# Optimization experiments

Measured on AMD Instinct MI355X. Metric: run time of the kernel, lower is better.

## Reference

```python
import jax, jax.numpy as jnp
import numpy as np

N = 50000      # nodes
E = 800000     # edges
F_IN = 128     # input node features
HID = 96       # hidden_channels (heads=1 -> in_dim=HID)
L = 4          # num_layers
OUT = 1
EPS_SM = 1e-16 # PyG softmax eps


def layer_norm(x, g, b):
    mu = jnp.mean(x, axis=-1, keepdims=True)
    var = jnp.var(x, axis=-1, keepdims=True)
    return (x - mu) * jax.lax.rsqrt(var + 1e-5) * g + b


def gatv2_layer(h, src, dst, ea, Wl, bl, Wr, br, We, att, bias):
    # GATv2Conv, heads=1, concat=True, add_self_loops=False, edge_dim=1
    xl = h @ Wl + bl                      # [N, C] source transform (x_j)
    xr = h @ Wr + br                      # [N, C] target transform (x_i)
    e = xl[src] + xr[dst] + ea @ We       # [E, C]
    e = jax.nn.leaky_relu(e, 0.2)
    alpha = e @ att                       # [E]
    # softmax over incoming edges of each destination node
    m = jax.ops.segment_max(alpha, dst, num_segments=N)
    a = jnp.exp(alpha - m[dst])
    s = jax.ops.segment_sum(a, dst, num_segments=N)
    a = a / (s[dst] + EPS_SM)
    out = jax.ops.segment_sum(xl[src] * a[:, None], dst, num_segments=N)
    return out + bias


def setup_inputs() -> dict:
    key = jax.random.key(0)
    ks = jax.random.split(key, 24)
    sc_in = 1.0 / np.sqrt(F_IN)
    sc_h = 1.0 / np.sqrt(HID)
    inp = {
        "x": jax.random.normal(ks[0], (N, F_IN), jnp.float32),
        "edge_index": jax.random.randint(ks[1], (2, E), 0, N, jnp.int64),
        "edge_weight": jax.random.uniform(ks[2], (E,), jnp.float32),
        "enc_W": jax.random.normal(ks[3], (F_IN, HID), jnp.float32) * sc_in,
        "enc_b": jnp.zeros((HID,), jnp.float32),
        "Wl": jax.random.normal(ks[4], (L, HID, HID), jnp.float32) * sc_h,
        "bl": jnp.zeros((L, HID), jnp.float32),
        "Wr": jax.random.normal(ks[5], (L, HID, HID), jnp.float32) * sc_h,
        "br": jnp.zeros((L, HID), jnp.float32),
        "We": jax.random.normal(ks[6], (L, 1, HID), jnp.float32),
        "att": jax.random.normal(ks[7], (L, HID), jnp.float32) * sc_h,
        "bias": jnp.zeros((L, HID), jnp.float32),
        "ln_g": jnp.ones((L, HID), jnp.float32),
        "ln_b": jnp.zeros((L, HID), jnp.float32),
        "lnf_g": jnp.ones((HID,), jnp.float32),
        "lnf_b": jnp.zeros((HID,), jnp.float32),
        "fc_W": jax.random.normal(ks[8], (HID, OUT), jnp.float32) * sc_h,
        "fc_b": jnp.zeros((OUT,), jnp.float32),
    }
    return inp


def reference(x, edge_index, edge_weight, enc_W, enc_b, Wl, bl, Wr, br, We, att,
              bias, ln_g, ln_b, lnf_g, lnf_b, fc_W, fc_b):
    src, dst = edge_index[0], edge_index[1]
    ea = edge_weight[:, None]             # [E, 1] edge_attr
    h = x @ enc_W + enc_b                 # node encoder
    for i in range(L):                    # DeepGCNLayer block='res+'
        hn = jax.nn.relu(layer_norm(h, ln_g[i], ln_b[i]))
        h = h + gatv2_layer(hn, src, dst, ea, Wl[i], bl[i], Wr[i], br[i],
                            We[i], att[i], bias[i])
    h = jax.nn.relu(layer_norm(h, lnf_g, lnf_b))
    return h @ fc_W + fc_b
```

## Files before the change

kernel.cpp:

```cpp
#include <hip/hip_runtime.h>
#include <math.h>

#define NN 50000
#define EE 800000
#define FIN 128
#define HID 96
#define NL 4
#define CHUNK 1024

typedef __attribute__((ext_vector_type(8))) short short8;
typedef __attribute__((ext_vector_type(4))) float floatx4;
typedef __attribute__((ext_vector_type(2))) _Float16 half2v;

__device__ __forceinline__ float wave_sum(float v) {
    #pragma unroll
    for (int off = 32; off > 0; off >>= 1) v += __shfl_xor(v, off);
    return v;
}

__device__ __forceinline__ unsigned short f32_to_bf16_rne(float x) {
    unsigned u = __float_as_uint(x);
    unsigned r = (u + 0x7FFFu + ((u >> 16) & 1u)) >> 16;
    return (unsigned short)r;
}
__device__ __forceinline__ float bf16_to_f32(unsigned short h) {
    return __uint_as_float(((unsigned)h) << 16);
}
__device__ __forceinline__ void split2(float a, float b, unsigned& hi, unsigned& lo) {
    unsigned short ha = f32_to_bf16_rne(a), hb = f32_to_bf16_rne(b);
    unsigned short la = f32_to_bf16_rne(a - bf16_to_f32(ha));
    unsigned short lb = f32_to_bf16_rne(b - bf16_to_f32(hb));
    hi = (unsigned)ha | ((unsigned)hb << 16);
    lo = (unsigned)la | ((unsigned)lb << 16);
}

__global__ void k_hist(const int* __restrict__ dst, int* __restrict__ deg, int E) {
    int e = blockIdx.x * blockDim.x + threadIdx.x;
    if (e < E) atomicAdd(&deg[dst[e]], 1);
}

__global__ void k_scan1(const int* __restrict__ deg, int* __restrict__ partials, int n) {
    __shared__ int lds[256];
    int t = threadIdx.x;
    int base = blockIdx.x * CHUNK + t * 4;
    int s = 0;
    #pragma unroll
    for (int q = 0; q < 4; q++) { int idx = base + q; if (idx < n) s += deg[idx]; }
    lds[t] = s; __syncthreads();
    for (int o = 128; o > 0; o >>= 1) { if (t < o) lds[t] += lds[t + o]; __syncthreads(); }
    if (t == 0) partials[blockIdx.x] = lds[0];
}

__global__ void k_scan_mid(int* partials, int nb, int* rowptr, int n) {
    int lane = threadIdx.x;
    int orig = (lane < nb) ? partials[lane] : 0;
    int v = orig;
    #pragma unroll
    for (int off = 1; off < 64; off <<= 1) {
        int u = __shfl_up(v, off);
        if (lane >= off) v += u;
    }
    if (lane < nb) partials[lane] = v - orig;
    if (lane == 63) rowptr[n] = v;
}

__global__ void k_scan3(const int* __restrict__ deg, const int* __restrict__ partials,
                        int* __restrict__ rowptr, int* __restrict__ cursor, int n) {
    __shared__ int lds[256];
    int t = threadIdx.x;
    int base = blockIdx.x * CHUNK + t * 4;
    int v[4];
    #pragma unroll
    for (int q = 0; q < 4; q++) { int idx = base + q; v[q] = (idx < n) ? deg[idx] : 0; }
    int tsum = v[0] + v[1] + v[2] + v[3];
    lds[t] = tsum; __syncthreads();
    for (int o = 1; o < 256; o <<= 1) {
        int add = (t >= o) ? lds[t - o] : 0;
        __syncthreads();
        lds[t] += add;
        __syncthreads();
    }
    int excl = lds[t] - tsum;
    int run = partials[blockIdx.x] + excl;
    #pragma unroll
    for (int q = 0; q < 4; q++) {
        int idx = base + q;
        if (idx < n) { rowptr[idx] = run; cursor[idx] = run; run += v[q]; }
    }
}

__global__ void k_scatter(const int* __restrict__ src, const int* __restrict__ dst,
                          const float* __restrict__ ew, int* __restrict__ cursor,
                          uint2* __restrict__ epack, int E) {
    int e = blockIdx.x * blockDim.x + threadIdx.x;
    if (e < E) {
        int p = atomicAdd(&cursor[dst[e]], 1);
        epack[p] = make_uint2((unsigned)src[e], __float_as_uint(ew[e]));
    }
}

__global__ void k_wprep(const float* __restrict__ Wl, const float* __restrict__ Wr,
                        unsigned short* __restrict__ wf_hi, unsigned short* __restrict__ wf_lo) {
    int t = blockIdx.x * blockDim.x + threadIdx.x;
    if (t >= NL * 2 * 9216) return;
    int within = t % 9216, pair = t / 9216;
    int lr = pair & 1, layer = pair >> 1;
    int j = within & 7;
    int lane = (within >> 3) & 63;
    int cs = within >> 9;
    int s = cs % 3, ct = cs / 3;
    int col = ct * 16 + (lane & 15);
    int k = s * 32 + (lane >> 4) * 8 + j;
    const float* W = (lr ? Wr : Wl) + (size_t)layer * HID * HID;
    float v = W[k * HID + col];
    unsigned short hi = f32_to_bf16_rne(v);
    wf_hi[t] = hi;
    wf_lo[t] = f32_to_bf16_rne(v - bf16_to_f32(hi));
}

__global__ void k_wprep_enc(const float* __restrict__ W,
                            unsigned short* __restrict__ we_hi, unsigned short* __restrict__ we_lo) {
    int t = blockIdx.x * blockDim.x + threadIdx.x;
    if (t >= 12288) return;
    int j = t & 7;
    int lane = (t >> 3) & 63;
    int cs = t >> 9;
    int s = cs & 3, ct = cs >> 2;
    int col = ct * 16 + (lane & 15);
    int k = s * 32 + (lane >> 4) * 8 + j;
    float v = W[k * HID + col];
    unsigned short hi = f32_to_bf16_rne(v);
    we_hi[t] = hi;
    we_lo[t] = f32_to_bf16_rne(v - bf16_to_f32(hi));
}

__global__ __launch_bounds__(256) void k_enc_mfma(const float* __restrict__ x,
        const unsigned short* __restrict__ we_hi, const unsigned short* __restrict__ we_lo,
        const float* __restrict__ b, float* __restrict__ h, int n) {
    int t = threadIdx.x;
    int wave = t >> 6, lane = t & 63;
    int quad = lane >> 4, lid = lane & 15;
    int r0 = blockIdx.x * 64 + wave * 16;
    int arow = r0 + lid; if (arow >= n) arow = n - 1;
    short8 aH[4], aL[4];
    #pragma unroll
    for (int s = 0; s < 4; s++) {
        float4 p0 = *(const float4*)(x + (size_t)arow * FIN + s * 32 + quad * 8);
        float4 p1 = *(const float4*)(x + (size_t)arow * FIN + s * 32 + quad * 8 + 4);
        float f[8] = {p0.x, p0.y, p0.z, p0.w, p1.x, p1.y, p1.z, p1.w};
        #pragma unroll
        for (int j = 0; j < 8; j++) {
            unsigned short hi = f32_to_bf16_rne(f[j]);
            aH[s][j] = (short)hi;
            aL[s][j] = (short)f32_to_bf16_rne(f[j] - bf16_to_f32(hi));
        }
    }
    #pragma unroll
    for (int ct = 0; ct < 6; ct++) {
        floatx4 acc = {0.f, 0.f, 0.f, 0.f};
        #pragma unroll
        for (int s = 0; s < 4; s++) {
            short8 bH = *(const short8*)(we_hi + ((ct * 4 + s) * 64 + lane) * 8);
            short8 bL = *(const short8*)(we_lo + ((ct * 4 + s) * 64 + lane) * 8);
            acc = __builtin_amdgcn_mfma_f32_16x16x32_bf16(aH[s], bH, acc, 0, 0, 0);
            acc = __builtin_amdgcn_mfma_f32_16x16x32_bf16(aH[s], bL, acc, 0, 0, 0);
            acc = __builtin_amdgcn_mfma_f32_16x16x32_bf16(aL[s], bH, acc, 0, 0, 0);
        }
        int col = ct * 16 + lid;
        float bv = b[col];
        #pragma unroll
        for (int rg = 0; rg < 4; rg++) {
            int orow = r0 + quad * 4 + rg;
            if (orow < n) h[(size_t)orow * HID + col] = acc[rg] + bv;
        }
    }
}

__global__ __launch_bounds__(256) void k_gemm2_mfma(
        const unsigned short* __restrict__ hn_hi, const unsigned short* __restrict__ hn_lo,
        const unsigned short* __restrict__ wf_hi, const unsigned short* __restrict__ wf_lo,
        const float* __restrict__ bl, const float* __restrict__ br,
        unsigned short* __restrict__ xl_h, float* __restrict__ xr, int n) {
    __shared__ unsigned short lh[9216];
    __shared__ unsigned short ll[9216];
    int t = threadIdx.x;
    int wave = t >> 6, lane = t & 63;
    int quad = lane >> 4, lid = lane & 15;
    int r0 = blockIdx.x * 64 + wave * 16;
    int arow = r0 + lid; if (arow >= n) arow = n - 1;
    short8 aH[3], aL[3];
    #pragma unroll
    for (int s = 0; s < 3; s++) {
        aH[s] = *(const short8*)(hn_hi + (size_t)arow * HID + s * 32 + quad * 8);
        aL[s] = *(const short8*)(hn_lo + (size_t)arow * HID + s * 32 + quad * 8);
    }
    for (int lr = 0; lr < 2; lr++) {
        const unsigned short* sh = wf_hi + lr * 9216;
        const unsigned short* sl = wf_lo + lr * 9216;
        __syncthreads();
        for (int u = t; u < 1152; u += 256) {
            *(short8*)(lh + u * 8) = *(const short8*)(sh + u * 8);
            *(short8*)(ll + u * 8) = *(const short8*)(sl + u * 8);
        }
        __syncthreads();
        const float* bias = lr ? br : bl;
        #pragma unroll
        for (int ct = 0; ct < 6; ct++) {
            floatx4 acc = {0.f, 0.f, 0.f, 0.f};
            #pragma unroll
            for (int s = 0; s < 3; s++) {
                short8 bH = *(const short8*)(lh + ((ct * 3 + s) * 64 + lane) * 8);
                short8 bL = *(const short8*)(ll + ((ct * 3 + s) * 64 + lane) * 8);
                acc = __builtin_amdgcn_mfma_f32_16x16x32_bf16(aH[s], bH, acc, 0, 0, 0);
                acc = __builtin_amdgcn_mfma_f32_16x16x32_bf16(aH[s], bL, acc, 0, 0, 0);
                acc = __builtin_amdgcn_mfma_f32_16x16x32_bf16(aL[s], bH, acc, 0, 0, 0);
            }
            int col = ct * 16 + lid;
            float bv = bias[col];
            #pragma unroll
            for (int rg = 0; rg < 4; rg++) {
                int orow = r0 + quad * 4 + rg;
                if (orow < n) {
                    float o = acc[rg] + bv;
                    if (lr == 0) {
                        _Float16 hv = (_Float16)o;
                        xl_h[(size_t)orow * HID + col] = *(unsigned short*)&hv;
                    } else {
                        xr[(size_t)orow * HID + col] = o;
                    }
                }
            }
        }
    }
}

__global__ __launch_bounds__(256) void k_ln_relu(const float* __restrict__ h, const float* __restrict__ g,
                                                 const float* __restrict__ bt,
                                                 unsigned short* __restrict__ hn_hi,
                                                 unsigned short* __restrict__ hn_lo, int n) {
    int lane = threadIdx.x & 63;
    int node = blockIdx.x * 4 + (threadIdx.x >> 6);
    if (node >= n) return;
    bool act = lane < 48;
    int d = lane * 2;
    float2 x2 = make_float2(0.f, 0.f);
    if (act) x2 = *(const float2*)(h + (size_t)node * HID + d);
    float s  = wave_sum(x2.x + x2.y);
    float sq = wave_sum(x2.x * x2.x + x2.y * x2.y);
    float mu = s * (1.f / 96.f);
    float var = sq * (1.f / 96.f) - mu * mu;
    float rs = rsqrtf(var + 1e-5f);
    if (act) {
        float2 g2 = *(const float2*)(g + d);
        float2 b2 = *(const float2*)(bt + d);
        float ox = fmaxf((x2.x - mu) * rs * g2.x + b2.x, 0.f);
        float oy = fmaxf((x2.y - mu) * rs * g2.y + b2.y, 0.f);
        unsigned hi, lo;
        split2(ox, oy, hi, lo);
        *(unsigned*)(hn_hi + (size_t)node * HID + d) = hi;
        *(unsigned*)(hn_lo + (size_t)node * HID + d) = lo;
    }
}

__global__ __launch_bounds__(256) void k_gat_fused(
        const unsigned short* __restrict__ xl_h, const float* __restrict__ xr,
        const uint2* __restrict__ ep, const int* __restrict__ rowptr,
        const float* __restrict__ We, const float* __restrict__ att, const float* __restrict__ bias,
        float* __restrict__ h,
        unsigned short* __restrict__ hn_hi, unsigned short* __restrict__ hn_lo,
        float* __restrict__ out_final,
        const float* __restrict__ g, const float* __restrict__ bt,
        const float* __restrict__ fcW, const float* __restrict__ fcb,
        int mode, int n) {
    int lane = threadIdx.x & 63;
    int node = blockIdx.x * 4 + (threadIdx.x >> 6);
    if (node >= n) return;
    int grp = lane >> 4, sub = lane & 15;
    bool act = sub < 12;
    int d0 = sub * 8;
    unsigned gOffB = (unsigned)((act ? sub : 11) * 16);

    half2v we_h[4], at_h[4], xr_h[4];
    if (act) {
        float4 a0 = *(const float4*)(We + d0),  a1 = *(const float4*)(We + d0 + 4);
        float4 c0 = *(const float4*)(att + d0), c1 = *(const float4*)(att + d0 + 4);
        float4 r0 = *(const float4*)(xr + (size_t)node * HID + d0);
        float4 r1 = *(const float4*)(xr + (size_t)node * HID + d0 + 4);
        we_h[0] = half2v{(_Float16)a0.x, (_Float16)a0.y}; we_h[1] = half2v{(_Float16)a0.z, (_Float16)a0.w};
        we_h[2] = half2v{(_Float16)a1.x, (_Float16)a1.y}; we_h[3] = half2v{(_Float16)a1.z, (_Float16)a1.w};
        at_h[0] = half2v{(_Float16)c0.x, (_Float16)c0.y}; at_h[1] = half2v{(_Float16)c0.z, (_Float16)c0.w};
        at_h[2] = half2v{(_Float16)c1.x, (_Float16)c1.y}; at_h[3] = half2v{(_Float16)c1.z, (_Float16)c1.w};
        xr_h[0] = half2v{(_Float16)r0.x, (_Float16)r0.y}; xr_h[1] = half2v{(_Float16)r0.z, (_Float16)r0.w};
        xr_h[2] = half2v{(_Float16)r1.x, (_Float16)r1.y}; xr_h[3] = half2v{(_Float16)r1.z, (_Float16)r1.w};
    } else {
        #pragma unroll
        for (int j = 0; j < 4; j++) {
            we_h[j] = half2v{(_Float16)0.f, (_Float16)0.f};
            at_h[j] = we_h[j]; xr_h[j] = we_h[j];
        }
    }
    const half2v c02 = half2v{(_Float16)0.2f, (_Float16)0.2f};

    int beg = rowptr[node], end = rowptr[node + 1];
    float ssum = 0.f;
    float acc[8];
    #pragma unroll
    for (int j = 0; j < 8; j++) acc[j] = 0.f;

    union U8 { uint4 u; half2v h2[4]; _Float16 hf[8]; };

    auto lq = [&](int p, uint4& vraw, float& w, bool& val) {
        int pe = p + grp;
        val = pe < end;
        int pc = val ? pe : end - 1;
        uint2 e = ep[pc];
        w = __uint_as_float(e.y);
        vraw = *(const uint4*)((const char*)xl_h + (e.x * 192u + gOffB));
    };
    auto proc = [&](const uint4& vraw, float w, bool val) {
        U8 cv; cv.u = vraw;
        _Float16 wh = (_Float16)w;
        half2v w2 = half2v{wh, wh};
        float q = 0.f;
        #pragma unroll
        for (int j = 0; j < 4; j++) {
            half2v t = cv.h2[j] + xr_h[j];
            t = w2 * we_h[j] + t;
            half2v t2 = t * c02;
            t = __builtin_elementwise_max(t, t2);
#if __has_builtin(__builtin_amdgcn_fdot2)
            q = __builtin_amdgcn_fdot2(t, at_h[j], q, false);
#else
            q = fmaf((float)t[0], (float)at_h[j][0], q);
            q = fmaf((float)t[1], (float)at_h[j][1], q);
#endif
        }
        q += __shfl_xor(q, 1); q += __shfl_xor(q, 2);
        q += __shfl_xor(q, 4); q += __shfl_xor(q, 8);
        float e = val ? __expf(q) : 0.f;
        ssum += e;
        #pragma unroll
        for (int j = 0; j < 8; j++) acc[j] = fmaf((float)cv.hf[j], e, acc[j]);
    };

    if (beg < end) {
        uint4 vA, vB; float wA, wB; bool okA, okB;
        lq(beg,     vA, wA, okA);
        lq(beg + 4, vB, wB, okB);
        for (int p = beg; p < end; p += 8) {
            proc(vA, wA, okA);
            lq(p + 8, vA, wA, okA);
            proc(vB, wB, okB);
            lq(p + 12, vB, wB, okB);
        }
    }

    ssum += __shfl_xor(ssum, 16); ssum += __shfl_xor(ssum, 32);
    #pragma unroll
    for (int j = 0; j < 8; j++) {
        acc[j] += __shfl_xor(acc[j], 16);
        acc[j] += __shfl_xor(acc[j], 32);
    }
    float inv = 1.f / (ssum + 1e-16f);

    float nh[8];
    float s1 = 0.f, s2 = 0.f;
    if (act) {
        float4 h0 = *(const float4*)(h + (size_t)node * HID + d0);
        float4 h1 = *(const float4*)(h + (size_t)node * HID + d0 + 4);
        float4 b0 = *(const float4*)(bias + d0);
        float4 b1 = *(const float4*)(bias + d0 + 4);
        float hv[8] = {h0.x,h0.y,h0.z,h0.w,h1.x,h1.y,h1.z,h1.w};
        float bv[8] = {b0.x,b0.y,b0.z,b0.w,b1.x,b1.y,b1.z,b1.w};
        #pragma unroll
        for (int j = 0; j < 8; j++) {
            nh[j] = hv[j] + acc[j] * inv + bv[j];
            s1 += nh[j];
            s2 += nh[j] * nh[j];
        }
    } else {
        #pragma unroll
        for (int j = 0; j < 8; j++) nh[j] = 0.f;
    }
    #pragma unroll
    for (int off = 1; off < 16; off <<= 1) {
        s1 += __shfl_xor(s1, off);
        s2 += __shfl_xor(s2, off);
    }
    float mu = s1 * (1.f / 96.f);
    float var = s2 * (1.f / 96.f) - mu * mu;
    float rs = rsqrtf(var + 1e-5f);

    if (mode == 0) {
        if (grp == 0 && act) {
            float4 g0 = *(const float4*)(g + d0),  g1 = *(const float4*)(g + d0 + 4);
            float4 t0 = *(const float4*)(bt + d0), t1 = *(const float4*)(bt + d0 + 4);
            float gv[8] = {g0.x,g0.y,g0.z,g0.w,g1.x,g1.y,g1.z,g1.w};
            float tv[8] = {t0.x,t0.y,t0.z,t0.w,t1.x,t1.y,t1.z,t1.w};
            *(float4*)(h + (size_t)node * HID + d0)     = make_float4(nh[0], nh[1], nh[2], nh[3]);
            *(float4*)(h + (size_t)node * HID + d0 + 4) = make_float4(nh[4], nh[5], nh[6], nh[7]);
            unsigned hi[4], lo[4];
            #pragma unroll
            for (int j = 0; j < 4; j++) {
                float ox = fmaxf((nh[2*j]   - mu) * rs * gv[2*j]   + tv[2*j],   0.f);
                float oy = fmaxf((nh[2*j+1] - mu) * rs * gv[2*j+1] + tv[2*j+1], 0.f);
                split2(ox, oy, hi[j], lo[j]);
            }
            *(uint4*)(hn_hi + (size_t)node * HID + d0) = make_uint4(hi[0], hi[1], hi[2], hi[3]);
            *(uint4*)(hn_lo + (size_t)node * HID + d0) = make_uint4(lo[0], lo[1], lo[2], lo[3]);
        }
    } else {
        float pacc = 0.f;
        if (act) {
            float4 g0 = *(const float4*)(g + d0),  g1 = *(const float4*)(g + d0 + 4);
            float4 t0 = *(const float4*)(bt + d0), t1 = *(const float4*)(bt + d0 + 4);
            float4 w0 = *(const float4*)(fcW + d0), w1 = *(const float4*)(fcW + d0 + 4);
            float gv[8] = {g0.x,g0.y,g0.z,g0.w,g1.x,g1.y,g1.z,g1.w};
            float tv[8] = {t0.x,t0.y,t0.z,t0.w,t1.x,t1.y,t1.z,t1.w};
            float wv[8] = {w0.x,w0.y,w0.z,w0.w,w1.x,w1.y,w1.z,w1.w};
            #pragma unroll
            for (int j = 0; j < 8; j++) {
                float y = fmaxf((nh[j] - mu) * rs * gv[j] + tv[j], 0.f);
                pacc = fmaf(y, wv[j], pacc);
            }
        }
        #pragma unroll
        for (int off = 1; off < 16; off <<= 1) pacc += __shfl_xor(pacc, off);
        if (lane == 0) out_final[node] = pacc + fcb[0];
    }
}

extern "C" void kernel_launch(void* const* d_in, const int* in_sizes, int n_in,
                              void* d_out, int out_size, void* d_ws, size_t ws_size,
                              hipStream_t stream) {
    const float* x    = (const float*)d_in[0];
    const int*   ei   = (const int*)  d_in[1];
    const float* ew   = (const float*)d_in[2];
    const float* encW = (const float*)d_in[3];
    const float* encB = (const float*)d_in[4];
    const float* Wl   = (const float*)d_in[5];
    const float* bl   = (const float*)d_in[6];
    const float* Wr   = (const float*)d_in[7];
    const float* br   = (const float*)d_in[8];
    const float* We   = (const float*)d_in[9];
    const float* att  = (const float*)d_in[10];
    const float* bias = (const float*)d_in[11];
    const float* lng  = (const float*)d_in[12];
    const float* lnb  = (const float*)d_in[13];
    const float* lnfg = (const float*)d_in[14];
    const float* lnfb = (const float*)d_in[15];
    const float* fcW  = (const float*)d_in[16];
    const float* fcb  = (const float*)d_in[17];
    float* out = (float*)d_out;

    const int* src = ei;
    const int* dst = ei + EE;

    char* ws = (char*)d_ws;
    size_t off = 0;
    auto alloc = [&](size_t bytes) -> void* {
        void* p = ws + off;
        off += (bytes + 255) & ~(size_t)255;
        return p;
    };
    float* h      = (float*)alloc((size_t)NN * HID * 4);
    float* xr     = (float*)alloc((size_t)NN * HID * 4);
    unsigned short* xl_h  = (unsigned short*)alloc((size_t)NN * HID * 2 + 256);
    unsigned short* hn_hi = (unsigned short*)alloc((size_t)NN * HID * 2);
    unsigned short* hn_lo = (unsigned short*)alloc((size_t)NN * HID * 2);
    unsigned short* wf_hi = (unsigned short*)alloc((size_t)NL * 2 * 9216 * 2);
    unsigned short* wf_lo = (unsigned short*)alloc((size_t)NL * 2 * 9216 * 2);
    unsigned short* we_hi = (unsigned short*)alloc(12288 * 2);
    unsigned short* we_lo = (unsigned short*)alloc(12288 * 2);
    int*   deg    = (int*)  alloc((size_t)NN * 4);
    int*   rowptr = (int*)  alloc((size_t)(NN + 1) * 4);
    int*   cursor = (int*)  alloc((size_t)NN * 4);
    uint2* epack  = (uint2*)alloc((size_t)EE * 8);
    int*   parts  = (int*)  alloc(256 * 4);

    const int NB = (NN + CHUNK - 1) / CHUNK;
    const int EB = (EE + 255) / 256;
    const int MB = (NN + 63) / 64;
    const int WB = (NN + 3) / 4;

    hipMemsetAsync(deg, 0, (size_t)NN * 4, stream);
    k_hist<<<EB, 256, 0, stream>>>(dst, deg, EE);
    k_scan1<<<NB, 256, 0, stream>>>(deg, parts, NN);
    k_scan_mid<<<1, 64, 0, stream>>>(parts, NB, rowptr, NN);
    k_scan3<<<NB, 256, 0, stream>>>(deg, parts, rowptr, cursor, NN);
    k_scatter<<<EB, 256, 0, stream>>>(src, dst, ew, cursor, epack, EE);

    k_wprep<<<(NL * 2 * 9216 + 255) / 256, 256, 0, stream>>>(Wl, Wr, wf_hi, wf_lo);
    k_wprep_enc<<<(12288 + 255) / 256, 256, 0, stream>>>(encW, we_hi, we_lo);

    k_enc_mfma<<<MB, 256, 0, stream>>>(x, we_hi, we_lo, encB, h, NN);
    k_ln_relu<<<WB, 256, 0, stream>>>(h, lng, lnb, hn_hi, hn_lo, NN);

    for (int l = 0; l < NL; l++) {
        k_gemm2_mfma<<<MB, 256, 0, stream>>>(hn_hi, hn_lo,
            wf_hi + (size_t)l * 2 * 9216, wf_lo + (size_t)l * 2 * 9216,
            bl + l * HID, br + l * HID, xl_h, xr, NN);
        if (l < NL - 1) {
            k_gat_fused<<<WB, 256, 0, stream>>>(xl_h, xr, epack, rowptr,
                We + l * HID, att + l * HID, bias + l * HID,
                h, hn_hi, hn_lo, (float*)nullptr,
                lng + (l + 1) * HID, lnb + (l + 1) * HID,
                (const float*)nullptr, (const float*)nullptr, 0, NN);
        } else {
            k_gat_fused<<<WB, 256, 0, stream>>>(xl_h, xr, epack, rowptr,
                We + l * HID, att + l * HID, bias + l * HID,
                h, (unsigned short*)nullptr, (unsigned short*)nullptr, out,
                lnfg, lnfb, fcW, fcb, 1, NN);
        }
    }
}
```

Before: 503.7 us.

## Fuse first LayerNorm into encoder GEMM, store xr in fp16, use exp2

Folds the first LayerNorm+ReLU and bf16 hi/lo split into the encoder MFMA epilogue, computing row stats with 16-lane shuffles and dropping the separate k_ln_relu launch and its re-read of h. The gemm now writes the target transform xr as fp16 rather than fp32, halving that buffer's write and read traffic, and the GAT kernel loads it with one 16-byte load. The attention vector is pre-scaled by log2(e) so the softmax can use exp2f. Risks are extra fp16 rounding on xr and scattered 2-byte stores in the fused encoder epilogue.

```diff
diff --git a/kernel.cpp b/kernel.cpp
--- a/kernel.cpp
+++ b/kernel.cpp
@@ -25,13 +25,6 @@
 }
 __device__ __forceinline__ float bf16_to_f32(unsigned short h) {
     return __uint_as_float(((unsigned)h) << 16);
-}
-__device__ __forceinline__ void split2(float a, float b, unsigned& hi, unsigned& lo) {
-    unsigned short ha = f32_to_bf16_rne(a), hb = f32_to_bf16_rne(b);
-    unsigned short la = f32_to_bf16_rne(a - bf16_to_f32(ha));
-    unsigned short lb = f32_to_bf16_rne(b - bf16_to_f32(hb));
-    hi = (unsigned)ha | ((unsigned)hb << 16);
-    lo = (unsigned)la | ((unsigned)lb << 16);
 }
 
 __global__ void k_hist(const int* __restrict__ dst, int* __restrict__ deg, int E) {
@@ -136,7 +129,10 @@
 
 __global__ __launch_bounds__(256) void k_enc_mfma(const float* __restrict__ x,
         const unsigned short* __restrict__ we_hi, const unsigned short* __restrict__ we_lo,
-        const float* __restrict__ b, float* __restrict__ h, int n) {
+        const float* __restrict__ b,
+        const float* __restrict__ lng, const float* __restrict__ lnb,
+        float* __restrict__ h,
+        unsigned short* __restrict__ hn_hi, unsigned short* __restrict__ hn_lo, int n) {
     int t = threadIdx.x;
     int wave = t >> 6, lane = t & 63;
     int quad = lane >> 4, lid = lane & 15;
@@ -155,6 +151,7 @@
             aL[s][j] = (short)f32_to_bf16_rne(f[j] - bf16_to_f32(hi));
         }
     }
+    floatx4 o[6];
     #pragma unroll
     for (int ct = 0; ct < 6; ct++) {
         floatx4 acc = {0.f, 0.f, 0.f, 0.f};
@@ -166,12 +163,35 @@
             acc = __builtin_amdgcn_mfma_f32_16x16x32_bf16(aH[s], bL, acc, 0, 0, 0);
             acc = __builtin_amdgcn_mfma_f32_16x16x32_bf16(aL[s], bH, acc, 0, 0, 0);
         }
-        int col = ct * 16 + lid;
-        float bv = b[col];
-        #pragma unroll
-        for (int rg = 0; rg < 4; rg++) {
-            int orow = r0 + quad * 4 + rg;
-            if (orow < n) h[(size_t)orow * HID + col] = acc[rg] + bv;
+        float bv = b[ct * 16 + lid];
+        #pragma unroll
+        for (int rg = 0; rg < 4; rg++) o[ct][rg] = acc[rg] + bv;
+    }
+    #pragma unroll
+    for (int rg = 0; rg < 4; rg++) {
+        float s1 = 0.f, s2 = 0.f;
+        #pragma unroll
+        for (int ct = 0; ct < 6; ct++) { s1 += o[ct][rg]; s2 += o[ct][rg] * o[ct][rg]; }
+        #pragma unroll
+        for (int off = 1; off < 16; off <<= 1) {
+            s1 += __shfl_xor(s1, off);
+            s2 += __shfl_xor(s2, off);
+        }
+        float mu = s1 * (1.f / 96.f);
+        float var = s2 * (1.f / 96.f) - mu * mu;
+        float rs = rsqrtf(var + 1e-5f);
+        int orow = r0 + quad * 4 + rg;
+        if (orow < n) {
+            #pragma unroll
+            for (int ct = 0; ct < 6; ct++) {
+                int col = ct * 16 + lid;
+                float v = o[ct][rg];
+                h[(size_t)orow * HID + col] = v;
+                float y = fmaxf((v - mu) * rs * lng[col] + lnb[col], 0.f);
+                unsigned short hi = f32_to_bf16_rne(y);
+                hn_hi[(size_t)orow * HID + col] = hi;
+                hn_lo[(size_t)orow * HID + col] = f32_to_bf16_rne(y - bf16_to_f32(hi));
+            }
         }
     }
 }
@@ -180,7 +200,7 @@
         const unsigned short* __restrict__ hn_hi, const unsigned short* __restrict__ hn_lo,
         const unsigned short* __restrict__ wf_hi, const unsigned short* __restrict__ wf_lo,
         const float* __restrict__ bl, const float* __restrict__ br,
-        unsigned short* __restrict__ xl_h, float* __restrict__ xr, int n) {
+        unsigned short* __restrict__ xl_h, unsigned short* __restrict__ xr_h, int n) {
     __shared__ unsigned short lh[9216];
     __shared__ unsigned short ll[9216];
     int t = threadIdx.x;
@@ -204,6 +224,7 @@
         }
         __syncthreads();
         const float* bias = lr ? br : bl;
+        unsigned short* out = lr ? xr_h : xl_h;
         #pragma unroll
         for (int ct = 0; ct < 6; ct++) {
             floatx4 acc = {0.f, 0.f, 0.f, 0.f};
@@ -221,49 +242,16 @@
             for (int rg = 0; rg < 4; rg++) {
                 int orow = r0 + quad * 4 + rg;
                 if (orow < n) {
-                    float o = acc[rg] + bv;
-                    if (lr == 0) {
-                        _Float16 hv = (_Float16)o;
-                        xl_h[(size_t)orow * HID + col] = *(unsigned short*)&hv;
-                    } else {
-                        xr[(size_t)orow * HID + col] = o;
-                    }
+                    _Float16 hv = (_Float16)(acc[rg] + bv);
+                    out[(size_t)orow * HID + col] = *(unsigned short*)&hv;
                 }
             }
         }
     }
 }
 
-__global__ __launch_bounds__(256) void k_ln_relu(const float* __restrict__ h, const float* __restrict__ g,
-                                                 const float* __restrict__ bt,
-                                                 unsigned short* __restrict__ hn_hi,
-                                                 unsigned short* __restrict__ hn_lo, int n) {
-    int lane = threadIdx.x & 63;
-    int node = blockIdx.x * 4 + (threadIdx.x >> 6);
-    if (node >= n) return;
-    bool act = lane < 48;
-    int d = lane * 2;
-    float2 x2 = make_float2(0.f, 0.f);
-    if (act) x2 = *(const float2*)(h + (size_t)node * HID + d);
-    float s  = wave_sum(x2.x + x2.y);
-    float sq = wave_sum(x2.x * x2.x + x2.y * x2.y);
-    float mu = s * (1.f / 96.f);
-    float var = sq * (1.f / 96.f) - mu * mu;
-    float rs = rsqrtf(var + 1e-5f);
-    if (act) {
-        float2 g2 = *(const float2*)(g + d);
-        float2 b2 = *(const float2*)(bt + d);
-        float ox = fmaxf((x2.x - mu) * rs * g2.x + b2.x, 0.f);
-        float oy = fmaxf((x2.y - mu) * rs * g2.y + b2.y, 0.f);
-        unsigned hi, lo;
-        split2(ox, oy, hi, lo);
-        *(unsigned*)(hn_hi + (size_t)node * HID + d) = hi;
-        *(unsigned*)(hn_lo + (size_t)node * HID + d) = lo;
-    }
-}
-
 __global__ __launch_bounds__(256) void k_gat_fused(
-        const unsigned short* __restrict__ xl_h, const float* __restrict__ xr,
+        const unsigned short* __restrict__ xl_h, const unsigned short* __restrict__ xr_h,
         const uint2* __restrict__ ep, const int* __restrict__ rowptr,
         const float* __restrict__ We, const float* __restrict__ att, const float* __restrict__ bias,
         float* __restrict__ h,
@@ -280,23 +268,29 @@
     int d0 = sub * 8;
     unsigned gOffB = (unsigned)((act ? sub : 11) * 16);
 
-    half2v we_h[4], at_h[4], xr_h[4];
-    if (act) {
-        float4 a0 = *(const float4*)(We + d0),  a1 = *(const float4*)(We + d0 + 4);
-        float4 c0 = *(const float4*)(att + d0), c1 = *(const float4*)(att + d0 + 4);
-        float4 r0 = *(const float4*)(xr + (size_t)node * HID + d0);
-        float4 r1 = *(const float4*)(xr + (size_t)node * HID + d0 + 4);
-        we_h[0] = half2v{(_Float16)a0.x, (_Float16)a0.y}; we_h[1] = half2v{(_Float16)a0.z, (_Float16)a0.w};
-        we_h[2] = half2v{(_Float16)a1.x, (_Float16)a1.y}; we_h[3] = half2v{(_Float16)a1.z, (_Float16)a1.w};
-        at_h[0] = half2v{(_Float16)c0.x, (_Float16)c0.y}; at_h[1] = half2v{(_Float16)c0.z, (_Float16)c0.w};
-        at_h[2] = half2v{(_Float16)c1.x, (_Float16)c1.y}; at_h[3] = half2v{(_Float16)c1.z, (_Float16)c1.w};
-        xr_h[0] = half2v{(_Float16)r0.x, (_Float16)r0.y}; xr_h[1] = half2v{(_Float16)r0.z, (_Float16)r0.w};
-        xr_h[2] = half2v{(_Float16)r1.x, (_Float16)r1.y}; xr_h[3] = half2v{(_Float16)r1.z, (_Float16)r1.w};
-    } else {
-        #pragma unroll
-        for (int j = 0; j < 4; j++) {
-            we_h[j] = half2v{(_Float16)0.f, (_Float16)0.f};
-            at_h[j] = we_h[j]; xr_h[j] = we_h[j];
+    const float LOG2E = 1.4426950408889634f;
+    half2v we_h[4], at_h[4], xr_hv[4];
+    {
+        union U8 { uint4 u; half2v h2[4]; };
+        U8 xrw;
+        xrw.u = *(const uint4*)((const char*)xr_h + ((unsigned)node * 192u + gOffB));
+        if (act) {
+            float4 a0 = *(const float4*)(We + d0),  a1 = *(const float4*)(We + d0 + 4);
+            float4 c0 = *(const float4*)(att + d0), c1 = *(const float4*)(att + d0 + 4);
+            we_h[0] = half2v{(_Float16)a0.x, (_Float16)a0.y}; we_h[1] = half2v{(_Float16)a0.z, (_Float16)a0.w};
+            we_h[2] = half2v{(_Float16)a1.x, (_Float16)a1.y}; we_h[3] = half2v{(_Float16)a1.z, (_Float16)a1.w};
+            at_h[0] = half2v{(_Float16)(c0.x*LOG2E), (_Float16)(c0.y*LOG2E)};
+            at_h[1] = half2v{(_Float16)(c0.z*LOG2E), (_Float16)(c0.w*LOG2E)};
+            at_h[2] = half2v{(_Float16)(c1.x*LOG2E), (_Float16)(c1.y*LOG2E)};
+            at_h[3] = half2v{(_Float16)(c1.z*LOG2E), (_Float16)(c1.w*LOG2E)};
+            #pragma unroll
+            for (int j = 0; j < 4; j++) xr_hv[j] = xrw.h2[j];
+        } else {
+            #pragma unroll
+            for (int j = 0; j < 4; j++) {
+                we_h[j] = half2v{(_Float16)0.f, (_Float16)0.f};
+                at_h[j] = we_h[j]; xr_hv[j] = we_h[j];
+            }
         }
     }
     const half2v c02 = half2v{(_Float16)0.2f, (_Float16)0.2f};
@@ -324,7 +318,7 @@
         float q = 0.f;
         #pragma unroll
         for (int j = 0; j < 4; j++) {
-            half2v t = cv.h2[j] + xr_h[j];
+            half2v t = cv.h2[j] + xr_hv[j];
             t = w2 * we_h[j] + t;
             half2v t2 = t * c02;
             t = __builtin_elementwise_max(t, t2);
@@ -337,7 +331,7 @@
         }
         q += __shfl_xor(q, 1); q += __shfl_xor(q, 2);
         q += __shfl_xor(q, 4); q += __shfl_xor(q, 8);
-        float e = val ? __expf(q) : 0.f;
+        float e = val ? exp2f(q) : 0.f;
         ssum += e;
         #pragma unroll
         for (int j = 0; j < 8; j++) acc[j] = fmaf((float)cv.hf[j], e, acc[j]);
@@ -404,7 +398,11 @@
             for (int j = 0; j < 4; j++) {
                 float ox = fmaxf((nh[2*j]   - mu) * rs * gv[2*j]   + tv[2*j],   0.f);
                 float oy = fmaxf((nh[2*j+1] - mu) * rs * gv[2*j+1] + tv[2*j+1], 0.f);
-                split2(ox, oy, hi[j], lo[j]);
+                unsigned short hx = f32_to_bf16_rne(ox), hy = f32_to_bf16_rne(oy);
+                unsigned short lx = f32_to_bf16_rne(ox - bf16_to_f32(hx));
+                unsigned short ly = f32_to_bf16_rne(oy - bf16_to_f32(hy));
+                hi[j] = (unsigned)hx | ((unsigned)hy << 16);
+                lo[j] = (unsigned)lx | ((unsigned)ly << 16);
             }
             *(uint4*)(hn_hi + (size_t)node * HID + d0) = make_uint4(hi[0], hi[1], hi[2], hi[3]);
             *(uint4*)(hn_lo + (size_t)node * HID + d0) = make_uint4(lo[0], lo[1], lo[2], lo[3]);
@@ -464,8 +462,8 @@
         return p;
     };
     float* h      = (float*)alloc((size_t)NN * HID * 4);
-    float* xr     = (float*)alloc((size_t)NN * HID * 4);
     unsigned short* xl_h  = (unsigned short*)alloc((size_t)NN * HID * 2 + 256);
+    unsigned short* xr_h  = (unsigned short*)alloc((size_t)NN * HID * 2 + 256);
     unsigned short* hn_hi = (unsigned short*)alloc((size_t)NN * HID * 2);
     unsigned short* hn_lo = (unsigned short*)alloc((size_t)NN * HID * 2);
     unsigned short* wf_hi = (unsigned short*)alloc((size_t)NL * 2 * 9216 * 2);
@@ -493,21 +491,20 @@
     k_wprep<<<(NL * 2 * 9216 + 255) / 256, 256, 0, stream>>>(Wl, Wr, wf_hi, wf_lo);
     k_wprep_enc<<<(12288 + 255) / 256, 256, 0, stream>>>(encW, we_hi, we_lo);
 
-    k_enc_mfma<<<MB, 256, 0, stream>>>(x, we_hi, we_lo, encB, h, NN);
-    k_ln_relu<<<WB, 256, 0, stream>>>(h, lng, lnb, hn_hi, hn_lo, NN);
+    k_enc_mfma<<<MB, 256, 0, stream>>>(x, we_hi, we_lo, encB, lng, lnb, h, hn_hi, hn_lo, NN);
 
     for (int l = 0; l < NL; l++) {
         k_gemm2_mfma<<<MB, 256, 0, stream>>>(hn_hi, hn_lo,
             wf_hi + (size_t)l * 2 * 9216, wf_lo + (size_t)l * 2 * 9216,
-            bl + l * HID, br + l * HID, xl_h, xr, NN);
+            bl + l * HID, br + l * HID, xl_h, xr_h, NN);
         if (l < NL - 1) {
-            k_gat_fused<<<WB, 256, 0, stream>>>(xl_h, xr, epack, rowptr,
+            k_gat_fused<<<WB, 256, 0, stream>>>(xl_h, xr_h, epack, rowptr,
                 We + l * HID, att + l * HID, bias + l * HID,
                 h, hn_hi, hn_lo, (float*)nullptr,
                 lng + (l + 1) * HID, lnb + (l + 1) * HID,
                 (const float*)nullptr, (const float*)nullptr, 0, NN);
         } else {
-            k_gat_fused<<<WB, 256, 0, stream>>>(xl_h, xr, epack, rowptr,
+            k_gat_fused<<<WB, 256, 0, stream>>>(xl_h, xr_h, epack, rowptr,
                 We + l * HID, att + l * HID, bias + l * HID,
                 h, (unsigned short*)nullptr, (unsigned short*)nullptr, out,
                 lnfg, lnfb, fcW, fcb, 1, NN);
```

After: 497.3 us. Within noise of the previous version (-1.3%).
